# Optimization experiments

Hardware: AMD Instinct MI355X
Metric: run time of the kernel (lower is better)

## Reference

```python
import jax, jax.numpy as jnp
import numpy as np

B, C, H, W = 2, 128, 128, 128
K, STRIDE, DIL, NH = 8, 2, 2, 8
HID = int(C * 4 / 3)  # 170


def _ln(x, g, b):
    # layernorm2d: normalize over channel axis (last axis in NHWC)
    mu = jnp.mean(x, axis=-1, keepdims=True)
    xc = x - mu
    var = jnp.mean(xc * xc, axis=-1, keepdims=True)
    return xc * jax.lax.rsqrt(var + 1e-6) * g + b


def _nat_attn(xn, qkv_w, qkv_b, qg, qb, kg, kb, proj_w, proj_b):
    # dilated/strided local-neighborhood attention (NATTEN-style)
    Bq, Hq, Wq, Cq = xn.shape
    dh = Cq // NH
    qkv = xn @ qkv_w.T + qkv_b
    q, k, v = jnp.split(qkv, 3, axis=-1)
    q = _ln(q, qg, qb)
    k = _ln(k, kg, kb)
    # keys/values on a stride-subsampled grid
    kc = k[:, ::STRIDE, ::STRIDE, :]
    vc = v[:, ::STRIDE, ::STRIDE, :]
    Hc, Wc = Hq // STRIDE, Wq // STRIDE
    plo = DIL * (K // 2)
    phi = DIL * (K - 1 - K // 2)
    pad = ((0, 0), (plo, phi), (plo, phi), (0, 0))
    kp = jnp.pad(kc, pad)
    vp = jnp.pad(vc, pad)
    mp = jnp.pad(jnp.ones((1, Hc, Wc, 1), dtype=bool), pad)
    offs = [(i * DIL, j * DIL) for i in range(K) for j in range(K)]  # fixed k*k window taps
    kn = jnp.stack([kp[:, a:a + Hc, b:b + Wc, :] for a, b in offs], axis=3).reshape(Bq, Hc, Wc, K * K, NH, dh)
    vn = jnp.stack([vp[:, a:a + Hc, b:b + Wc, :] for a, b in offs], axis=3).reshape(Bq, Hc, Wc, K * K, NH, dh)
    mn = jnp.stack([mp[:, a:a + Hc, b:b + Wc, 0] for a, b in offs], axis=3)  # [1,Hc,Wc,kk]
    # each full-res query maps to its coarse kv cell: [B,Hc,stride,Wc,stride,heads,dh]
    q6 = q.reshape(Bq, Hc, STRIDE, Wc, STRIDE, NH, dh)
    scores = jnp.einsum('bisjtnd,bijknd->bisjtnk', q6, kn) * (dh ** -0.5)
    m = mn[:, :, None, :, None, None, :]
    scores = jnp.where(m, scores, jnp.float32(-1e30))
    attn = jax.nn.softmax(scores, axis=-1)
    out = jnp.einsum('bisjtnk,bijknd->bisjtnd', attn, vn).reshape(Bq, Hq, Wq, Cq)
    return out @ proj_w.T + proj_b


def _cffn(xn, fc1_w, fc1_b, mg, mb, fc2_w, fc2_b):
    h = xn @ fc1_w.T + fc1_b
    h = _ln(h, mg, mb)
    h = jax.nn.gelu(h, approximate=True)  # gelu_tanh
    return h @ fc2_w.T + fc2_b


def setup_inputs():
    key = jax.random.key(0)
    ks = jax.random.split(key, 6)
    w = lambda k, shp: jax.random.normal(k, shp, dtype=jnp.float32) * 0.02
    z = lambda n: jnp.zeros((n,), jnp.float32)
    o = lambda n: jnp.ones((n,), jnp.float32)
    return {
        'x': jax.random.normal(ks[0], (B, C, H, W), dtype=jnp.float32),
        'qkv_w': w(ks[1], (3 * C, C)), 'qkv_b': z(3 * C),
        'qg': o(C), 'qb': z(C), 'kg': o(C), 'kb': z(C),
        'proj_w': w(ks[2], (C, C)), 'proj_b': z(C),
        'n1g': o(C), 'n1b': z(C), 'n2g': o(C), 'n2b': z(C),
        'ls1_g': jnp.full((C,), 1e-5, jnp.float32),
        'ls2_g': jnp.full((C,), 1e-5, jnp.float32),
        'fc1_w': w(ks[3], (HID, C)), 'fc1_b': z(HID),
        'mg': o(HID), 'mb': z(HID),
        'fc2_w': w(ks[4], (C, HID)), 'fc2_b': z(C),
    }


def reference(x, qkv_w, qkv_b, qg, qb, kg, kb, proj_w, proj_b, n1g, n1b, n2g, n2b, ls1_g, ls2_g, fc1_w, fc1_b, mg, mb, fc2_w, fc2_b):
    xh = jnp.transpose(x, (0, 2, 3, 1))  # NCHW -> NHWC
    xh = xh + ls1_g * _nat_attn(_ln(xh, n1g, n1b), qkv_w, qkv_b, qg, qb, kg, kb, proj_w, proj_b)
    xh = xh + ls2_g * _cffn(_ln(xh, n2g, n2b), fc1_w, fc1_b, mg, mb, fc2_w, fc2_b)
    return jnp.transpose(xh, (0, 3, 1, 2))
```

## Files before the change

kernel.cpp:

```cpp
#include <hip/hip_runtime.h>
#include <hip/hip_bf16.h>

typedef __hip_bfloat16 BF;
typedef __attribute__((ext_vector_type(8))) short bf16x8;
typedef __attribute__((ext_vector_type(4))) float f32x4;


#define ASTR 200
#define KSTR 136

__device__ __forceinline__ unsigned cvt2(float lo, float hi){
  unsigned r;
  asm("v_cvt_pk_bf16_f32 %0, %1, %2" : "=v"(r) : "v"(lo), "v"(hi));
  return r;
}
__device__ __forceinline__ bf16x8 pk8(float4 a, float4 b){
  union{ unsigned u[4]; bf16x8 v; } c;
  c.u[0] = cvt2(a.x, a.y); c.u[1] = cvt2(a.z, a.w);
  c.u[2] = cvt2(b.x, b.y); c.u[3] = cvt2(b.z, b.w);
  return c.v;
}

__device__ __forceinline__ void gsum16h(float v[16], float* red, int tid){
  #pragma unroll
  for(int s = 1; s < 64; s <<= 1){
    #pragma unroll
    for(int i = 0; i < 16; i++) v[i] += __shfl_xor(v[i], s);
  }
  const int wid = tid >> 6, half = tid >> 7;
  __syncthreads();
  if((tid & 63) == 0){
    #pragma unroll
    for(int i = 0; i < 16; i++) red[wid*16 + i] = v[i];
  }
  __syncthreads();
  #pragma unroll
  for(int i = 0; i < 16; i++) v[i] = red[half*32 + i] + red[half*32 + 16 + i];
}

__device__ __forceinline__ void rowredh(float s1[4], float s2[4], float* red, int tid){
  const int lane = tid & 63, wid = tid >> 6, half = tid >> 7;
  #pragma unroll
  for(int m = 1; m < 16; m <<= 1){
    #pragma unroll
    for(int r = 0; r < 4; r++){ s1[r] += __shfl_xor(s1[r], m); s2[r] += __shfl_xor(s2[r], m); }
  }
  const int q4 = lane >> 4;
  __syncthreads();
  if((lane & 15) == 0){
    #pragma unroll
    for(int r = 0; r < 4; r++){
      red[wid*32 + q4*4 + r]      = s1[r];
      red[wid*32 + 16 + q4*4 + r] = s2[r];
    }
  }
  __syncthreads();
  #pragma unroll
  for(int r = 0; r < 4; r++){
    s1[r] = red[half*64 + q4*4 + r]      + red[half*64 + 32 + q4*4 + r];
    s2[r] = red[half*64 + 16 + q4*4 + r] + red[half*64 + 48 + q4*4 + r];
  }
}

__device__ __forceinline__ void rowred4(float s1[4], float s2[4], float* red,
                                        int wave, int lane){
  #pragma unroll
  for(int m = 1; m < 16; m <<= 1){
    #pragma unroll
    for(int r = 0; r < 4; r++){ s1[r] += __shfl_xor(s1[r], m); s2[r] += __shfl_xor(s2[r], m); }
  }
  const int q4 = lane >> 4;
  __syncthreads();
  if((lane & 15) == 0){
    #pragma unroll
    for(int r = 0; r < 4; r++){
      red[wave*32 + q4*4 + r]      = s1[r];
      red[wave*32 + 16 + q4*4 + r] = s2[r];
    }
  }
  __syncthreads();
  #pragma unroll
  for(int r = 0; r < 4; r++){
    s1[r] = red[q4*4 + r] + red[32 + q4*4 + r] + red[64 + q4*4 + r] + red[96 + q4*4 + r];
    s2[r] = red[16 + q4*4 + r] + red[48 + q4*4 + r] + red[80 + q4*4 + r] + red[112 + q4*4 + r];
  }
}

__global__ void __launch_bounds__(256)
k_pre(const float* __restrict__ x,
      const float* __restrict__ qkv_w, const float* __restrict__ proj_w,
      const float* __restrict__ fc1_w, const float* __restrict__ fc2_w,
      const float* __restrict__ qkv_b,
      const float* __restrict__ kg, const float* __restrict__ kb,
      const float* __restrict__ n1g, const float* __restrict__ n1b,
      BF* __restrict__ pk,
      float* __restrict__ kcb, float* __restrict__ vcbT){
  __shared__ __align__(16) unsigned char sm[9216];
  const int bx = blockIdx.x, tid = threadIdx.x;

  if(bx >= 512){
    const int idx = (bx - 512) * 256 + tid;
    if(idx < 112640){
      float val;
      if(idx < 49152){
        const int reg = idx >> 14, l = idx & 16383;
        const int j = l & 7, q = (l>>3)&3, n = (l>>5)&127, s = l>>12;
        val = qkv_w[(reg*128 + n)*128 + (s*32 + q*8 + j)];
      } else if(idx < 65536){
        const int l = idx - 49152;
        const int j = l&7, q=(l>>3)&3, n=(l>>5)&127, s=l>>12;
        val = proj_w[n*128 + (s*32+q*8+j)];
      } else if(idx < 88064){
        const int l = idx - 65536;
        const int j = l&7, q=(l>>3)&3, rem = l>>5;
        const int n = rem % 176, s = rem / 176;
        const int k = s*32+q*8+j;
        val = (n < 170) ? fc1_w[n*128 + k] : 0.f;
      } else {
        const int l = idx - 88064;
        const int j = l&7, q=(l>>3)&3, n=(l>>5)&127, s=l>>12;
        const int k = s*32+q*8+j;
        val = (k < 170) ? fc2_w[n*170 + k] : 0.f;
      }
      pk[idx] = __float2bfloat16(val);
    }
    for(int z = (bx - 512)*256 + tid; z < 262144; z += 440*256){
      const int bpr = z >> 10;
      const int pc  = (z >> 7) & 7;
      const int d   = z & 127;
      const int rjh5 = (pc < 5) ? pc : (32 + pc);
      vcbT[((size_t)bpr*40 + rjh5)*128 + d] = 0.f;
    }
    return;
  }

  BF* const Abuf = (BF*)sm;
  float* const red = (float*)(sm + 8704);
  const int lane = tid & 63, half = tid >> 7, wh = (tid >> 6) & 1, c = tid & 127;
  const int l15 = lane & 15, q4 = lane >> 4;
  const int cp0 = bx * 16;
  const int b = cp0 >> 12, ic = (cp0 & 4095) >> 6, jb = cp0 & 63;
  BF* const AbufH = Abuf + half*16*KSTR;

  float xv[8];
  {
    const size_t off = (size_t)(b*128 + c)*16384 + (size_t)(2*ic)*128 + 2*(jb + half*8);
    const float4* xp4 = (const float4*)(x + off);
    const float4 f0 = xp4[0], f1 = xp4[1], f2 = xp4[2], f3 = xp4[3];
    xv[0]=f0.x; xv[1]=f0.z; xv[2]=f1.x; xv[3]=f1.z;
    xv[4]=f2.x; xv[5]=f2.z; xv[6]=f3.x; xv[7]=f3.z;
  }
  float st[16];
  #pragma unroll
  for(int r = 0; r < 8; r++){ st[r] = xv[r]; st[8+r] = xv[r]*xv[r]; }
  gsum16h(st, red, tid);
  {
    const float g = n1g[c], be = n1b[c];
    #pragma unroll
    for(int r = 0; r < 8; r++){
      const float mu = st[r]*(1.f/128.f);
      const float var = st[8+r]*(1.f/128.f) - mu*mu;
      AbufH[r*KSTR + c] = __float2bfloat16((xv[r]-mu)*rsqrtf(var+1e-6f)*g + be);
    }
  }
  __syncthreads();
  bf16x8 af[4];
  #pragma unroll
  for(int s = 0; s < 4; s++) af[s] = *(const bf16x8*)&AbufH[l15*KSTR + s*32 + q4*8];

  f32x4 acc[4];
  #pragma unroll
  for(int nt = 0; nt < 4; nt++){ acc[nt][0]=0.f; acc[nt][1]=0.f; acc[nt][2]=0.f; acc[nt][3]=0.f; }
  #pragma unroll
  for(int nt = 0; nt < 4; nt++){
    const int n = (wh*4+nt)*16 + l15;
    #pragma unroll
    for(int s = 0; s < 4; s++){
      const float* wp = qkv_w + (size_t)(128 + n)*128 + s*32 + q4*8;
      acc[nt] = __builtin_amdgcn_mfma_f32_16x16x32_bf16(
        af[s], pk8(*(const float4*)wp, *(const float4*)(wp+4)), acc[nt], 0,0,0);
    }
  }
  float s1[4], s2[4];
  #pragma unroll
  for(int r = 0; r < 4; r++){ s1[r]=0.f; s2[r]=0.f; }
  #pragma unroll
  for(int nt = 0; nt < 4; nt++){
    const float colb = qkv_b[128 + (wh*4+nt)*16 + l15];
    #pragma unroll
    for(int r = 0; r < 4; r++){
      const float vv = acc[nt][r] + colb;
      acc[nt][r] = vv; s1[r] += vv; s2[r] += vv*vv;
    }
  }
  rowredh(s1, s2, red, tid);
  #pragma unroll
  for(int nt = 0; nt < 4; nt++){
    const int col = (wh*4+nt)*16 + l15;
    const float g = kg[col], be = kb[col];
    #pragma unroll
    for(int r = 0; r < 4; r++){
      const int row = q4*4 + r;
      if(row < 8){
        const float mu = s1[r]*(1.f/128.f);
        const float var = s2[r]*(1.f/128.f) - mu*mu;
        kcb[(size_t)(cp0 + half*8 + row)*128 + col] = (acc[nt][r]-mu)*rsqrtf(var+1e-6f)*g + be;
      }
    }
  }
  #pragma unroll
  for(int nt = 0; nt < 4; nt++){ acc[nt][0]=0.f; acc[nt][1]=0.f; acc[nt][2]=0.f; acc[nt][3]=0.f; }
  #pragma unroll
  for(int nt = 0; nt < 4; nt++){
    const int n = (wh*4+nt)*16 + l15;
    #pragma unroll
    for(int s = 0; s < 4; s++){
      const float* wp = qkv_w + (size_t)(256 + n)*128 + s*32 + q4*8;
      acc[nt] = __builtin_amdgcn_mfma_f32_16x16x32_bf16(
        af[s], pk8(*(const float4*)wp, *(const float4*)(wp+4)), acc[nt], 0,0,0);
    }
  }
  #pragma unroll
  for(int nt = 0; nt < 4; nt++){
    const int col = (wh*4+nt)*16 + l15;
    const float bv = qkv_b[256 + col];
    #pragma unroll
    for(int r = 0; r < 4; r++){
      const int row = q4*4 + r;
      if(row < 8){
        const int cp = cp0 + half*8 + row;
        const int b2 = cp >> 12, rr = cp & 4095;
        const int ri = rr >> 6, rj = rr & 63;
        vcbT[((((size_t)(b2*2 + (rj&1))*64 + ri)*40) + (rj>>1) + 5)*128 + col]
          = acc[nt][r] + bv;
      }
    }
  }
}

__global__ void __launch_bounds__(256, 6)
k_cell(const float* __restrict__ x,
       const BF* __restrict__ packQ, const BF* __restrict__ packP,
       const BF* __restrict__ packF1, const BF* __restrict__ packF2,
       const float* __restrict__ qkv_b,
       const float* __restrict__ qg, const float* __restrict__ qb,
       const float* __restrict__ n1g, const float* __restrict__ n1b,
       const float* __restrict__ proj_b,
       const float* __restrict__ ls1, const float* __restrict__ ls2,
       const float* __restrict__ n2g, const float* __restrict__ n2b,
       const float* __restrict__ fc1_b,
       const float* __restrict__ mg, const float* __restrict__ mb,
       const float* __restrict__ fc2_b,
       const float* __restrict__ kcb, const float* __restrict__ vcbT,
       float* __restrict__ out){
  __shared__ __align__(16) BF uni[4608];
  BF* const Abuf = uni;
  __shared__ float xvL[2048];
  __shared__ __align__(16) ushort qnH[2176];
  __shared__ ushort cidx2[256];
  float* const red = (float*)qnH;
  const int tid = threadIdx.x, wave = tid>>6, lane = tid&63;
  const int l15 = lane & 15, q4 = lane >> 4;

  const int bx0 = blockIdx.x;
  const int bx = ((bx0 & 7) << 8) | (bx0 >> 3);
  const int b = bx >> 10, rem = bx & 1023, ip = rem >> 5, jq = rem & 31;
  const int c = tid & 127, half = tid >> 7;

  float xv[8];
  {
    const size_t xb = (size_t)(b*128 + c)*16384 + (size_t)(4*ip + 2*half)*128 + 4*jq;
    const float4 r0 = *(const float4*)(x + xb);
    const float4 r1 = *(const float4*)(x + xb + 128);
    xv[0]=r0.x; xv[1]=r0.y; xv[2]=r0.z; xv[3]=r0.w;
    xv[4]=r1.x; xv[5]=r1.y; xv[6]=r1.z; xv[7]=r1.w;
    #pragma unroll
    for(int r = 0; r < 8; r++) xvL[(half*8 + r)*128 + c] = xv[r];
  }
  {
    const int cell = tid >> 6, e = tid & 63;
    const int i = e >> 3, j = e & 7;
    const int ic = 2*ip + (cell>>1), jcc = 2*jq + (cell&1);
    const int ri = ic + 2*i - 8, rj = jcc + 2*j - 8;
    const bool ok = (rj >= 0) && (rj < 64) && (ri >= 0) && (ri < 64);
    cidx2[cell*64 + e] = ok ? (ushort)(b*4096 + ri*64 + rj) : (ushort)0;
  }

  float st[16];
  #pragma unroll
  for(int r = 0; r < 8; r++){ st[r] = xv[r]; st[8+r] = xv[r]*xv[r]; }
  gsum16h(st, red, tid);
  {
    const float g = n1g[c], be = n1b[c];
    #pragma unroll
    for(int r = 0; r < 8; r++){
      const int p = half*8 + r;
      const float mu = st[r]*(1.f/128.f);
      const float var = st[8+r]*(1.f/128.f) - mu*mu;
      Abuf[p*ASTR + c] = __float2bfloat16((xv[r]-mu)*rsqrtf(var+1e-6f)*g + be);
    }
  }
  __syncthreads();

  {
    bf16x8 af[4];
    #pragma unroll
    for(int s = 0; s < 4; s++) af[s] = *(const bf16x8*)&Abuf[l15*ASTR + s*32 + q4*8];
    f32x4 acc[2];
    #pragma unroll
    for(int nt = 0; nt < 2; nt++){ acc[nt][0]=0.f; acc[nt][1]=0.f; acc[nt][2]=0.f; acc[nt][3]=0.f; }
    #pragma unroll
    for(int nt = 0; nt < 2; nt++){
      const int n = (wave*2+nt)*16 + l15;
      #pragma unroll
      for(int s = 0; s < 4; s++){
        bf16x8 bf = *(const bf16x8*)&packQ[((s*128 + n)*4 + q4)*8];
        acc[nt] = __builtin_amdgcn_mfma_f32_16x16x32_bf16(af[s], bf, acc[nt], 0,0,0);
      }
    }
    float s1[4], s2[4];
    #pragma unroll
    for(int r = 0; r < 4; r++){ s1[r]=0.f; s2[r]=0.f; }
    #pragma unroll
    for(int nt = 0; nt < 2; nt++){
      const float cb2 = qkv_b[(wave*2+nt)*16 + l15];
      #pragma unroll
      for(int r = 0; r < 4; r++){
        const float vv = acc[nt][r] + cb2;
        acc[nt][r] = vv; s1[r] += vv; s2[r] += vv*vv;
      }
    }
    rowred4(s1, s2, red, wave, lane);
    ushort tw[2][4];
    {
      float mu[4], rs[4];
      #pragma unroll
      for(int r = 0; r < 4; r++){
        mu[r] = s1[r]*(1.f/128.f);
        rs[r] = rsqrtf(s2[r]*(1.f/128.f) - mu[r]*mu[r] + 1e-6f);
      }
      #pragma unroll
      for(int nt = 0; nt < 2; nt++){
        const int col = (wave*2+nt)*16 + l15;
        const float g = qg[col], be = qb[col];
        float v0 = (acc[nt][0]-mu[0])*rs[0]*g + be;
        float v1 = (acc[nt][1]-mu[1])*rs[1]*g + be;
        float v2 = (acc[nt][2]-mu[2])*rs[2]*g + be;
        float v3 = (acc[nt][3]-mu[3])*rs[3]*g + be;
        const unsigned d0 = cvt2(v0, v1), d1 = cvt2(v2, v3);
        tw[nt][0] = (ushort)d0; tw[nt][1] = (ushort)(d0 >> 16);
        tw[nt][2] = (ushort)d1; tw[nt][3] = (ushort)(d1 >> 16);
      }
    }
    __syncthreads();
    #pragma unroll
    for(int nt = 0; nt < 2; nt++){
      const int col = (wave*2+nt)*16 + l15;
      const int colp = col + (col >> 4);
      #pragma unroll
      for(int r = 0; r < 4; r++){
        const int cell = 2*(q4>>1) + ((r>>1)&1);
        const int lp   = 2*(q4&1) + (r&1);
        qnH[cell*544 + colp*4 + lp] = tw[nt][r];
      }
    }
  }
  __syncthreads();

  const int hsub = l15 >> 2, px = l15 & 3;
  const int par4 = q4 >> 1, dbase = (q4 & 1) * 8;
  BF* const attw = uni + wave*1152;
  ushort* const Pb = (ushort*)attw;
  const ushort* cidx = cidx2 + wave*64;
  const ushort* qp = qnH + wave*544;
  const int ic = 2*ip + (wave>>1), jcc = 2*jq + (wave&1);
  const int i0 = l15 >> 3;
  const int rj = jcc + 2*(l15 & 7) - 8;
  const bool vj = (rj >= 0) && (rj < 64);
  float madd[4];
  #pragma unroll
  for(int nt = 0; nt < 4; nt++){
    const int ri = ic + 2*(nt*2 + i0) - 8;
    madd[nt] = (vj && ri >= 0 && ri < 64) ? 0.f : -1e30f;
  }
  const int parv = jcc & 1;
  const int riA = min(63, max(0, ic + 2*q4 - 8));
  const int riB = min(63, max(0, ic + 2*q4));
  const float* vbA = vcbT + ((((size_t)(b*2 + parv)*64 + riA)*40) + (jcc>>1) + 1)*128 + l15;
  const float* vbB = vcbT + ((((size_t)(b*2 + parv)*64 + riB)*40) + (jcc>>1) + 1)*128 + l15;

  f32x4 oC[2];
  #pragma unroll
  for(int hg = 0; hg < 2; hg++){
    bf16x8 afq0, afq1;
    {
      const int idx0 = (hg*64 + hsub*16 + dbase + (hg*4 + hsub))*4 + px;
      short bq[8];
      #pragma unroll
      for(int j = 0; j < 8; j++) bq[j] = (short)qp[idx0 + 4*j];
      const bool a0 = (par4 == hsub), a1 = ((2 + par4) == hsub);
      #pragma unroll
      for(int j = 0; j < 8; j++){
        afq0[j] = a0 ? bq[j] : (short)0;
        afq1[j] = a1 ? bq[j] : (short)0;
      }
    }
    f32x4 accq[4];
    #pragma unroll
    for(int nt = 0; nt < 4; nt++){ accq[nt][0]=0.f; accq[nt][1]=0.f; accq[nt][2]=0.f; accq[nt][3]=0.f; }
    #pragma unroll
    for(int nt = 0; nt < 4; nt++){
      const float* kp = kcb + ((size_t)cidx[nt*16 + l15] << 7) + hg*64 + q4*8;
      const float4 k00 = *(const float4*)kp;
      const float4 k01 = *(const float4*)(kp + 4);
      const float4 k10 = *(const float4*)(kp + 32);
      const float4 k11 = *(const float4*)(kp + 36);
      accq[nt] = __builtin_amdgcn_mfma_f32_16x16x32_bf16(afq0, pk8(k00,k01), accq[nt], 0,0,0);
      accq[nt] = __builtin_amdgcn_mfma_f32_16x16x32_bf16(afq1, pk8(k10,k11), accq[nt], 0,0,0);
    }
    float inv[4];
    #pragma unroll
    for(int reg = 0; reg < 4; reg++){
      const float s0 = accq[0][reg]*0.25f + madd[0];
      const float s1 = accq[1][reg]*0.25f + madd[1];
      const float s2 = accq[2][reg]*0.25f + madd[2];
      const float s3 = accq[3][reg]*0.25f + madd[3];
      float m = fmaxf(fmaxf(s0,s1), fmaxf(s2,s3));
      #pragma unroll
      for(int sft = 1; sft < 16; sft <<= 1) m = fmaxf(m, __shfl_xor(m, sft));
      const float e0 = __expf(s0-m), e1 = __expf(s1-m);
      const float e2 = __expf(s2-m), e3 = __expf(s3-m);
      ushort* pr = Pb + (q4*4 + reg)*72 + l15;
      const unsigned d0 = cvt2(e0, e1), d1 = cvt2(e2, e3);
      pr[0]  = (ushort)d0;
      pr[16] = (ushort)(d0 >> 16);
      pr[32] = (ushort)d1;
      pr[48] = (ushort)(d1 >> 16);
      float es = e0+e1+e2+e3;
      #pragma unroll
      for(int sft = 1; sft < 16; sft <<= 1) es += __shfl_xor(es, sft);
      inv[reg] = 1.f/es;
    }
    const bf16x8 pa0 = *(const bf16x8*)(Pb + l15*72 + q4*8);
    const bf16x8 pa1 = *(const bf16x8*)(Pb + l15*72 + 32 + q4*8);

    f32x4 oSel; oSel[0]=0.f; oSel[1]=0.f; oSel[2]=0.f; oSel[3]=0.f;
    #pragma unroll
    for(int hs = 0; hs < 4; hs++){
      const int hoff = (hg*4 + hs)*16;
      float a0[8], a1[8];
      #pragma unroll
      for(int j = 0; j < 8; j++){
        a0[j] = vbA[j*128 + hoff];
        a1[j] = vbB[j*128 + hoff];
      }
      union{ unsigned u[4]; bf16x8 v; } c0, c1;
      c0.u[0]=cvt2(a0[0],a0[1]); c0.u[1]=cvt2(a0[2],a0[3]);
      c0.u[2]=cvt2(a0[4],a0[5]); c0.u[3]=cvt2(a0[6],a0[7]);
      c1.u[0]=cvt2(a1[0],a1[1]); c1.u[1]=cvt2(a1[2],a1[3]);
      c1.u[2]=cvt2(a1[4],a1[5]); c1.u[3]=cvt2(a1[6],a1[7]);
      f32x4 accv; accv[0]=0.f; accv[1]=0.f; accv[2]=0.f; accv[3]=0.f;
      accv = __builtin_amdgcn_mfma_f32_16x16x32_bf16(pa0, c0.v, accv, 0,0,0);
      accv = __builtin_amdgcn_mfma_f32_16x16x32_bf16(pa1, c1.v, accv, 0,0,0);
      if(q4 == hs){ oSel[0]=accv[0]; oSel[1]=accv[1]; oSel[2]=accv[2]; oSel[3]=accv[3]; }
    }
    oC[hg][0] = oSel[0]*inv[0]; oC[hg][1] = oSel[1]*inv[1];
    oC[hg][2] = oSel[2]*inv[2]; oC[hg][3] = oSel[3]*inv[3];
  }
  __syncthreads();
  {
    ushort* ab = (ushort*)Abuf;
    #pragma unroll
    for(int hg = 0; hg < 2; hg++){
      const int col = (hg*4 + q4)*16 + l15;
      const unsigned d0 = cvt2(oC[hg][0], oC[hg][1]);
      const unsigned d1 = cvt2(oC[hg][2], oC[hg][3]);
      const ushort ov[4] = {(ushort)d0, (ushort)(d0>>16), (ushort)d1, (ushort)(d1>>16)};
      #pragma unroll
      for(int reg = 0; reg < 4; reg++){
        const int row_p = 8*(wave>>1) + 4*(reg>>1) + 2*(wave&1) + (reg&1);
        ab[row_p*ASTR + col] = ov[reg];
      }
    }
  }
  __syncthreads();

  float xh[2][4];
  {
    bf16x8 af[4];
    #pragma unroll
    for(int s = 0; s < 4; s++) af[s] = *(const bf16x8*)&Abuf[l15*ASTR + s*32 + q4*8];
    f32x4 acc[2];
    #pragma unroll
    for(int nt = 0; nt < 2; nt++){ acc[nt][0]=0.f; acc[nt][1]=0.f; acc[nt][2]=0.f; acc[nt][3]=0.f; }
    #pragma unroll
    for(int nt = 0; nt < 2; nt++){
      const int n = (wave*2+nt)*16 + l15;
      #pragma unroll
      for(int s = 0; s < 4; s++){
        bf16x8 bf = *(const bf16x8*)&packP[((s*128 + n)*4 + q4)*8];
        acc[nt] = __builtin_amdgcn_mfma_f32_16x16x32_bf16(af[s], bf, acc[nt], 0,0,0);
      }
    }
    float s1[4], s2[4];
    #pragma unroll
    for(int r = 0; r < 4; r++){ s1[r]=0.f; s2[r]=0.f; }
    #pragma unroll
    for(int nt = 0; nt < 2; nt++){
      const int col = (wave*2+nt)*16 + l15;
      const float bp = proj_b[col], l1 = ls1[col];
      #pragma unroll
      for(int r = 0; r < 4; r++){
        const int p = q4*4 + r;
        const float hx = xvL[p*128 + col] + l1*(acc[nt][r] + bp);
        xh[nt][r] = hx; s1[r] += hx; s2[r] += hx*hx;
      }
    }
    rowred4(s1, s2, red, wave, lane);
    #pragma unroll
    for(int nt = 0; nt < 2; nt++){
      const int col = (wave*2+nt)*16 + l15;
      const float g2 = n2g[col], be = n2b[col];
      #pragma unroll
      for(int r = 0; r < 4; r++){
        const int p = q4*4 + r;
        const float mu = s1[r]*(1.f/128.f);
        const float var = s2[r]*(1.f/128.f) - mu*mu;
        Abuf[p*ASTR + col] =
          __float2bfloat16((xh[nt][r]-mu)*rsqrtf(var+1e-6f)*g2 + be);
      }
    }
  }
  __syncthreads();

  {
    bf16x8 af[4];
    #pragma unroll
    for(int s = 0; s < 4; s++) af[s] = *(const bf16x8*)&Abuf[l15*ASTR + s*32 + q4*8];
    const int NT1 = (wave < 3) ? 3 : 2;
    const int tb  = (wave < 3) ? wave*3 : 9;
    f32x4 acc1[3];
    #pragma unroll
    for(int nt = 0; nt < 3; nt++){ acc1[nt][0]=0.f; acc1[nt][1]=0.f; acc1[nt][2]=0.f; acc1[nt][3]=0.f; }
    for(int nt = 0; nt < NT1; nt++){
      const int n = (tb + nt)*16 + l15;
      #pragma unroll
      for(int s = 0; s < 4; s++){
        bf16x8 bf = *(const bf16x8*)&packF1[((s*176 + n)*4 + q4)*8];
        acc1[nt] = __builtin_amdgcn_mfma_f32_16x16x32_bf16(af[s], bf, acc1[nt], 0,0,0);
      }
    }
    float s1[4], s2[4];
    #pragma unroll
    for(int r = 0; r < 4; r++){ s1[r]=0.f; s2[r]=0.f; }
    for(int nt = 0; nt < NT1; nt++){
      const int col = (tb + nt)*16 + l15;
      const float b1 = (col < 170) ? fc1_b[col] : 0.f;
      #pragma unroll
      for(int r = 0; r < 4; r++){
        const float vv = acc1[nt][r] + b1;
        acc1[nt][r] = vv; s1[r] += vv; s2[r] += vv*vv;
      }
    }
    rowred4(s1, s2, red, wave, lane);
    for(int z = tid; z < 352; z += 256){
      const int row = z / 22, colz = 170 + (z - (z/22)*22);
      Abuf[row*ASTR + colz] = __float2bfloat16(0.f);
    }
    const float kA = 0.7978845608028654f, kB = 0.044715f;
    for(int nt = 0; nt < NT1; nt++){
      const int col = (tb + nt)*16 + l15;
      if(col < 170){
        const float g2 = mg[col], be = mb[col];
        #pragma unroll
        for(int r = 0; r < 4; r++){
          const int p = q4*4 + r;
          const float mu = s1[r]*(1.f/170.f);
          const float var = s2[r]*(1.f/170.f) - mu*mu;
          const float hn = (acc1[nt][r]-mu)*rsqrtf(var+1e-6f)*g2 + be;
          const float u = kA*(hn + kB*hn*hn*hn);
          const float gl = hn / (1.f + __expf(-2.f*u));
          Abuf[p*ASTR + col] = __float2bfloat16(gl);
        }
      }
    }
  }
  __syncthreads();

  {
    bf16x8 af[6];
    #pragma unroll
    for(int s = 0; s < 6; s++) af[s] = *(const bf16x8*)&Abuf[l15*ASTR + s*32 + q4*8];
    f32x4 acc[2];
    #pragma unroll
    for(int nt = 0; nt < 2; nt++){ acc[nt][0]=0.f; acc[nt][1]=0.f; acc[nt][2]=0.f; acc[nt][3]=0.f; }
    #pragma unroll
    for(int nt = 0; nt < 2; nt++){
      const int n = (wave*2+nt)*16 + l15;
      #pragma unroll
      for(int s = 0; s < 6; s++){
        bf16x8 bf = *(const bf16x8*)&packF2[((s*128 + n)*4 + q4)*8];
        acc[nt] = __builtin_amdgcn_mfma_f32_16x16x32_bf16(af[s], bf, acc[nt], 0,0,0);
      }
    }
    #pragma unroll
    for(int nt = 0; nt < 2; nt++){
      const int col = (wave*2+nt)*16 + l15;
      const float bf2 = fc2_b[col], l2 = ls2[col];
      float4 o4;
      o4.x = xh[nt][0] + l2*(acc[nt][0] + bf2);
      o4.y = xh[nt][1] + l2*(acc[nt][1] + bf2);
      o4.z = xh[nt][2] + l2*(acc[nt][2] + bf2);
      o4.w = xh[nt][3] + l2*(acc[nt][3] + bf2);
      *(float4*)(out + (size_t)(b*128 + col)*16384 + (size_t)(4*ip + q4)*128 + 4*jq) = o4;
    }
  }
}

extern "C" void kernel_launch(void* const* d_in, const int* in_sizes, int n_in,
                              void* d_out, int out_size, void* d_ws, size_t ws_size,
                              hipStream_t stream){
  const float* x      = (const float*)d_in[0];
  const float* qkv_w  = (const float*)d_in[1];
  const float* qkv_b  = (const float*)d_in[2];
  const float* qg     = (const float*)d_in[3];
  const float* qb     = (const float*)d_in[4];
  const float* kg     = (const float*)d_in[5];
  const float* kb     = (const float*)d_in[6];
  const float* proj_w = (const float*)d_in[7];
  const float* proj_b = (const float*)d_in[8];
  const float* n1g    = (const float*)d_in[9];
  const float* n1b    = (const float*)d_in[10];
  const float* n2g    = (const float*)d_in[11];
  const float* n2b    = (const float*)d_in[12];
  const float* ls1    = (const float*)d_in[13];
  const float* ls2    = (const float*)d_in[14];
  const float* fc1_w  = (const float*)d_in[15];
  const float* fc1_b  = (const float*)d_in[16];
  const float* mg     = (const float*)d_in[17];
  const float* mb     = (const float*)d_in[18];
  const float* fc2_w  = (const float*)d_in[19];
  const float* fc2_b  = (const float*)d_in[20];

  float* ws   = (float*)d_ws;
  float* kcb  = ws;
  float* vcbT = ws + 1048576;
  BF* pk      = (BF*)(ws + 3670016);
  BF* packQ   = pk;
  BF* packP   = pk + 49152;
  BF* packF1  = pk + 65536;
  BF* packF2  = pk + 88064;

  k_pre <<<952, 256, 0, stream>>>(x, qkv_w, proj_w, fc1_w, fc2_w, qkv_b,
                                  kg, kb, n1g, n1b, pk, kcb, vcbT);
  k_cell<<<2048, 256, 0, stream>>>(x, packQ, packP, packF1, packF2,
                                   qkv_b, qg, qb, n1g, n1b, proj_b, ls1, ls2,
                                   n2g, n2b, fc1_b, mg, mb, fc2_b,
                                   kcb, vcbT, (float*)d_out);
}
```

Baseline: 212.2 us.

## Store coarse K/V in bf16 with transposed V layout for vector loads

The intermediate coarse key and value buffers written by the pre-kernel change from fp32 to bf16. V is staged through shared memory and written in a d-major layout with padded columns, so the attention kernel can load eight contiguous bf16 values per lane directly as MFMA operands instead of gathering eight strided floats and converting them. This halves intermediate traffic and removes the per-use conversion work. In exchange it adds an extra shared-memory pass and barrier in the pre-kernel, a block index swizzle, and rounds K/V to bf16 earlier.

```diff
diff --git a/kernel.cpp b/kernel.cpp
--- a/kernel.cpp
+++ b/kernel.cpp
@@ -13,6 +13,9 @@
   unsigned r;
   asm("v_cvt_pk_bf16_f32 %0, %1, %2" : "=v"(r) : "v"(lo), "v"(hi));
   return r;
+}
+__device__ __forceinline__ ushort bf1(float f){
+  return (ushort)cvt2(f, f);
 }
 __device__ __forceinline__ bf16x8 pk8(float4 a, float4 b){
   union{ unsigned u[4]; bf16x8 v; } c;
@@ -94,12 +97,12 @@
       const float* __restrict__ kg, const float* __restrict__ kb,
       const float* __restrict__ n1g, const float* __restrict__ n1b,
       BF* __restrict__ pk,
-      float* __restrict__ kcb, float* __restrict__ vcbT){
+      BF* __restrict__ kcb, BF* __restrict__ vcbT){
   __shared__ __align__(16) unsigned char sm[9216];
-  const int bx = blockIdx.x, tid = threadIdx.x;
-
-  if(bx >= 512){
-    const int idx = (bx - 512) * 256 + tid;
+  const int bx0 = blockIdx.x, tid = threadIdx.x;
+
+  if(bx0 >= 512){
+    const int idx = (bx0 - 512) * 256 + tid;
     if(idx < 112640){
       float val;
       if(idx < 49152){
@@ -124,17 +127,17 @@
       }
       pk[idx] = __float2bfloat16(val);
     }
-    for(int z = (bx - 512)*256 + tid; z < 262144; z += 440*256){
-      const int bpr = z >> 10;
-      const int pc  = (z >> 7) & 7;
-      const int d   = z & 127;
-      const int rjh5 = (pc < 5) ? pc : (32 + pc);
-      vcbT[((size_t)bpr*40 + rjh5)*128 + d] = 0.f;
+    if(idx < 65536){
+      const int row = idx >> 1, side = idx & 1;
+      uint4 z; z.x = 0u; z.y = 0u; z.z = 0u; z.w = 0u;
+      *(uint4*)(vcbT + (size_t)row*48 + side*40) = z;
     }
     return;
   }
 
+  const int bx = ((bx0 & 7) << 6) | (bx0 >> 3);
   BF* const Abuf = (BF*)sm;
+  ushort* const vbuf = (ushort*)sm;
   float* const red = (float*)(sm + 8704);
   const int lane = tid & 63, half = tid >> 7, wh = (tid >> 6) & 1, c = tid & 127;
   const int l15 = lane & 15, q4 = lane >> 4;
@@ -204,7 +207,8 @@
       if(row < 8){
         const float mu = s1[r]*(1.f/128.f);
         const float var = s2[r]*(1.f/128.f) - mu*mu;
-        kcb[(size_t)(cp0 + half*8 + row)*128 + col] = (acc[nt][r]-mu)*rsqrtf(var+1e-6f)*g + be;
+        ((ushort*)kcb)[(size_t)(cp0 + half*8 + row)*128 + col] =
+          bf1((acc[nt][r]-mu)*rsqrtf(var+1e-6f)*g + be);
       }
     }
   }
@@ -220,6 +224,7 @@
         af[s], pk8(*(const float4*)wp, *(const float4*)(wp+4)), acc[nt], 0,0,0);
     }
   }
+  __syncthreads();
   #pragma unroll
   for(int nt = 0; nt < 4; nt++){
     const int col = (wh*4+nt)*16 + l15;
@@ -227,14 +232,17 @@
     #pragma unroll
     for(int r = 0; r < 4; r++){
       const int row = q4*4 + r;
-      if(row < 8){
-        const int cp = cp0 + half*8 + row;
-        const int b2 = cp >> 12, rr = cp & 4095;
-        const int ri = rr >> 6, rj = rr & 63;
-        vcbT[((((size_t)(b2*2 + (rj&1))*64 + ri)*40) + (rj>>1) + 5)*128 + col]
-          = acc[nt][r] + bv;
-      }
-    }
+      if(row < 8)
+        vbuf[(half*8 + row)*128 + col] = bf1(acc[nt][r] + bv);
+    }
+  }
+  __syncthreads();
+  {
+    const int par = tid >> 7, d = tid & 127;
+    union{ ushort s[8]; uint4 q; } w;
+    #pragma unroll
+    for(int j = 0; j < 8; j++) w.s[j] = vbuf[(2*j + par)*128 + d];
+    *(uint4*)(vcbT + ((((size_t)(b*2 + par)*64 + ic)*128) + d)*48 + (jb>>1) + 8) = w.q;
   }
 }
 
@@ -251,7 +259,7 @@
        const float* __restrict__ fc1_b,
        const float* __restrict__ mg, const float* __restrict__ mb,
        const float* __restrict__ fc2_b,
-       const float* __restrict__ kcb, const float* __restrict__ vcbT,
+       const BF* __restrict__ kcb, const BF* __restrict__ vcbT,
        float* __restrict__ out){
   __shared__ __align__(16) BF uni[4608];
   BF* const Abuf = uni;
@@ -386,8 +394,8 @@
   const int parv = jcc & 1;
   const int riA = min(63, max(0, ic + 2*q4 - 8));
   const int riB = min(63, max(0, ic + 2*q4));
-  const float* vbA = vcbT + ((((size_t)(b*2 + parv)*64 + riA)*40) + (jcc>>1) + 1)*128 + l15;
-  const float* vbB = vcbT + ((((size_t)(b*2 + parv)*64 + riB)*40) + (jcc>>1) + 1)*128 + l15;
+  const BF* vbA = vcbT + ((((size_t)(b*2 + parv)*64 + riA)*128) + l15)*48 + (jcc>>1) + 4;
+  const BF* vbB = vcbT + ((((size_t)(b*2 + parv)*64 + riB)*128) + l15)*48 + (jcc>>1) + 4;
 
   f32x4 oC[2];
   #pragma unroll
@@ -410,13 +418,12 @@
     for(int nt = 0; nt < 4; nt++){ accq[nt][0]=0.f; accq[nt][1]=0.f; accq[nt][2]=0.f; accq[nt][3]=0.f; }
     #pragma unroll
     for(int nt = 0; nt < 4; nt++){
-      const float* kp = kcb + ((size_t)cidx[nt*16 + l15] << 7) + hg*64 + q4*8;
-      const float4 k00 = *(const float4*)kp;
-      const float4 k01 = *(const float4*)(kp + 4);
-      const float4 k10 = *(const float4*)(kp + 32);
-      const float4 k11 = *(const float4*)(kp + 36);
-      accq[nt] = __builtin_amdgcn_mfma_f32_16x16x32_bf16(afq0, pk8(k00,k01), accq[nt], 0,0,0);
-      accq[nt] = __builtin_amdgcn_mfma_f32_16x16x32_bf16(afq1, pk8(k10,k11), accq[nt], 0,0,0);
+      const ushort* kp = (const ushort*)kcb + ((size_t)cidx[nt*16 + l15] << 7) + hg*64 + q4*8;
+      bf16x8 b0, b1;
+      __builtin_memcpy(&b0, kp, 16);
+      __builtin_memcpy(&b1, kp + 32, 16);
+      accq[nt] = __builtin_amdgcn_mfma_f32_16x16x32_bf16(afq0, b0, accq[nt], 0,0,0);
+      accq[nt] = __builtin_amdgcn_mfma_f32_16x16x32_bf16(afq1, b1, accq[nt], 0,0,0);
     }
     float inv[4];
     #pragma unroll
@@ -448,20 +455,12 @@
     #pragma unroll
     for(int hs = 0; hs < 4; hs++){
       const int hoff = (hg*4 + hs)*16;
-      float a0[8], a1[8];
-      #pragma unroll
-      for(int j = 0; j < 8; j++){
-        a0[j] = vbA[j*128 + hoff];
-        a1[j] = vbB[j*128 + hoff];
-      }
-      union{ unsigned u[4]; bf16x8 v; } c0, c1;
-      c0.u[0]=cvt2(a0[0],a0[1]); c0.u[1]=cvt2(a0[2],a0[3]);
-      c0.u[2]=cvt2(a0[4],a0[5]); c0.u[3]=cvt2(a0[6],a0[7]);
-      c1.u[0]=cvt2(a1[0],a1[1]); c1.u[1]=cvt2(a1[2],a1[3]);
-      c1.u[2]=cvt2(a1[4],a1[5]); c1.u[3]=cvt2(a1[6],a1[7]);
+      bf16x8 c0, c1;
+      __builtin_memcpy(&c0, vbA + (size_t)hoff*48, 16);
+      __builtin_memcpy(&c1, vbB + (size_t)hoff*48, 16);
       f32x4 accv; accv[0]=0.f; accv[1]=0.f; accv[2]=0.f; accv[3]=0.f;
-      accv = __builtin_amdgcn_mfma_f32_16x16x32_bf16(pa0, c0.v, accv, 0,0,0);
-      accv = __builtin_amdgcn_mfma_f32_16x16x32_bf16(pa1, c1.v, accv, 0,0,0);
+      accv = __builtin_amdgcn_mfma_f32_16x16x32_bf16(pa0, c0, accv, 0,0,0);
+      accv = __builtin_amdgcn_mfma_f32_16x16x32_bf16(pa1, c1, accv, 0,0,0);
       if(q4 == hs){ oSel[0]=accv[0]; oSel[1]=accv[1]; oSel[2]=accv[2]; oSel[3]=accv[3]; }
     }
     oC[hg][0] = oSel[0]*inv[0]; oC[hg][1] = oSel[1]*inv[1];
@@ -643,9 +642,9 @@
   const float* fc2_b  = (const float*)d_in[20];
 
   float* ws   = (float*)d_ws;
-  float* kcb  = ws;
-  float* vcbT = ws + 1048576;
-  BF* pk      = (BF*)(ws + 3670016);
+  BF* kcb     = (BF*)ws;
+  BF* vcbT    = (BF*)(ws + 524288);
+  BF* pk      = (BF*)(ws + 2097152);
   BF* packQ   = pk;
   BF* packP   = pk + 49152;
   BF* packF1  = pk + 65536;
```

New measurement: 197.8 us. 1.07x faster.
